# Performance work log

Hardware: AMD Instinct MI355X
Metric: run time of the kernel (lower is better)

The kernel has to match this reference:

```python
import jax, jax.numpy as jnp
import numpy as np

B, C, H, P, DIM, DEPTH, HEADS, MLP, NCLS = 32, 3, 224, 16, 768, 12, 12, 3072, 1000
HD = DIM // HEADS
GRID = H // P  # 14
SEQ = GRID * GRID + 1  # 197
EPS = 1e-6


def _ln(x, g, b):
    m = jnp.mean(x, axis=-1, keepdims=True)
    v = jnp.mean((x - m) ** 2, axis=-1, keepdims=True)
    return (x - m) * jax.lax.rsqrt(v + EPS) * g + b


def setup_inputs() -> dict:
    key = jax.random.key(0)
    ks = jax.random.split(key, 8)
    s = 0.02
    return {
        "img": jax.random.normal(ks[0], (B, C, H, H), dtype=jnp.float32),
        "conv_w": jax.random.normal(ks[1], (DIM, C, P, P), dtype=jnp.float32) * s,
        "conv_b": jnp.zeros((DIM,), jnp.float32),
        "cls_token": jnp.zeros((1, 1, DIM), jnp.float32),
        "pos_emb": jax.random.normal(ks[2], (1, SEQ, DIM), dtype=jnp.float32) * s,
        "ln1_g": jnp.ones((DEPTH, DIM), jnp.float32),
        "ln1_b": jnp.zeros((DEPTH, DIM), jnp.float32),
        "qkv_w": jax.random.normal(ks[3], (DEPTH, 3 * DIM, DIM), dtype=jnp.float32) * s,
        "qkv_b": jnp.zeros((DEPTH, 3 * DIM), jnp.float32),
        "out_w": jax.random.normal(ks[4], (DEPTH, DIM, DIM), dtype=jnp.float32) * s,
        "out_b": jnp.zeros((DEPTH, DIM), jnp.float32),
        "ln2_g": jnp.ones((DEPTH, DIM), jnp.float32),
        "ln2_b": jnp.zeros((DEPTH, DIM), jnp.float32),
        "mlp_w1": jax.random.normal(ks[5], (DEPTH, MLP, DIM), dtype=jnp.float32) * s,
        "mlp_b1": jnp.zeros((DEPTH, MLP), jnp.float32),
        "mlp_w2": jax.random.normal(ks[6], (DEPTH, DIM, MLP), dtype=jnp.float32) * s,
        "mlp_b2": jnp.zeros((DEPTH, DIM), jnp.float32),
        "lnf_g": jnp.ones((DIM,), jnp.float32),
        "lnf_b": jnp.zeros((DIM,), jnp.float32),
        "fc_w": jax.random.normal(ks[7], (NCLS, DIM), dtype=jnp.float32) * s,
        "fc_b": jnp.zeros((NCLS,), jnp.float32),
    }


def reference(img, conv_w, conv_b, cls_token, pos_emb, ln1_g, ln1_b, qkv_w, qkv_b,
              out_w, out_b, ln2_g, ln2_b, mlp_w1, mlp_b1, mlp_w2, mlp_b2,
              lnf_g, lnf_b, fc_w, fc_b):
    b = img.shape[0]
    # Patch embedding: Conv2d(k=P, s=P) == non-overlapping patch matmul.
    patches = img.reshape(b, C, GRID, P, GRID, P)
    x = jnp.einsum('bchpwq,dcpq->bhwd', patches, conv_w).reshape(b, GRID * GRID, DIM) + conv_b
    # prepend CLS, add positional embedding (dropout = identity at eval).
    cls = jnp.broadcast_to(cls_token, (b, 1, DIM))
    x = jnp.concatenate([cls, x], axis=1) + pos_emb[:, :SEQ]

    scale = 1.0 / jnp.sqrt(jnp.float32(HD))

    def layer(x, p):
        g1, b1, qw, qb, ow, ob, g2, b2, w1, bb1, w2, bb2 = p
        h = _ln(x, g1, b1)
        qkv = h @ qw.T + qb                                   # [b,s,3*dim]
        qkv = qkv.reshape(b, SEQ, 3, HEADS, HD)
        q, k, v = [jnp.transpose(qkv[:, :, i], (0, 2, 1, 3)) for i in range(3)]  # [b,h,s,d]
        attn = jax.nn.softmax(jnp.einsum('bhsd,bhtd->bhst', q, k) * scale, axis=-1)
        o = jnp.einsum('bhst,bhtd->bhsd', attn, v)
        o = jnp.transpose(o, (0, 2, 1, 3)).reshape(b, SEQ, DIM)
        x = x + (o @ ow.T + ob)
        h = _ln(x, g2, b2)
        m = jax.nn.gelu(h @ w1.T + bb1, approximate=False) @ w2.T + bb2
        return x + m, None

    x, _ = jax.lax.scan(layer, x, (ln1_g, ln1_b, qkv_w, qkv_b, out_w, out_b,
                                   ln2_g, ln2_b, mlp_w1, mlp_b1, mlp_w2, mlp_b2))
    x = _ln(x, lnf_g, lnf_b)
    return x[:, 0] @ fc_w.T + fc_b
```

## Files before the change

### kernel.cpp

```cpp
#include <hip/hip_runtime.h>
#include <math.h>

#define B_     32
#define SEQ_   197
#define DIM_   768
#define HEADS_ 12
#define HD_    64
#define MLP_   3072
#define NCLS_  1000
#define DEPTH_ 12
#define MROWS  (B_ * SEQ_)
#define MPAD   6400

#define WOFF_QKV 0
#define WOFF_OUT 1769472
#define WOFF_M1  2359296
#define WOFF_M2  4718592
#define LW_      7077888

typedef short s8v __attribute__((ext_vector_type(8)));
typedef float f4v __attribute__((ext_vector_type(4)));

__device__ __forceinline__ unsigned short f2bf(float f) {
    union { float f; unsigned u; } v; v.f = f;
    unsigned r = v.u + 0x7FFFu + ((v.u >> 16) & 1u);
    return (unsigned short)(r >> 16);
}
__device__ __forceinline__ float bf2f(unsigned short h) {
    union { unsigned u; float f; } v; v.u = ((unsigned)h) << 16; return v.f;
}
__device__ __forceinline__ void async16(const void* g, void* l) {
    __builtin_amdgcn_global_load_lds(
        (const __attribute__((address_space(1))) void*)g,
        (__attribute__((address_space(3))) void*)l, 16, 0, 0);
}

enum { EPI_QKV = 0, EPI_RES = 1, EPI_GELU = 2 };

template <int EPI, bool WB>
__global__ __launch_bounds__(256)
void gemm_bf16(const unsigned short* __restrict__ A, const void* __restrict__ Wv,
               const float* __restrict__ bias, float* __restrict__ X,
               unsigned short* __restrict__ O, int M, int N, int K,
               unsigned short* __restrict__ qo, unsigned short* __restrict__ ko,
               unsigned short* __restrict__ vo) {
    __shared__ __align__(16) unsigned short As[128 * 64];
    __shared__ __align__(16) unsigned short Bs[128 * 64];
    const int tid = threadIdx.x;
    const int m0 = blockIdx.y * 128, n0 = blockIdx.x * 128;
    const int w = tid >> 6, lane = tid & 63;
    const int wm = w & 1, wn = w >> 1;
    const int qd = lane >> 4, mr = lane & 15;

    f4v acc[4][4] = {};

    for (int k0 = 0; k0 < K; k0 += 64) {
#pragma unroll
        for (int r = 0; r < 4; r++) {
            int c = r * 256 + tid;
            int m = c >> 3, slot = c & 7;
            int j = slot ^ (m & 7);
            async16(A + (size_t)(m0 + m) * K + k0 + j * 8, (char*)As + c * 16);
        }
        if constexpr (WB) {
            const unsigned short* Wb = (const unsigned short*)Wv;
#pragma unroll
            for (int r = 0; r < 4; r++) {
                int c = r * 256 + tid;
                int n = c >> 3, slot = c & 7;
                int j = slot ^ (n & 7);
                async16(Wb + (size_t)(n0 + n) * K + k0 + j * 8, (char*)Bs + c * 16);
            }
        } else {
            const float* Wf = (const float*)Wv;
#pragma unroll
            for (int r = 0; r < 8; r++) {
                int u = r * 256 + tid;
                int n = u >> 4, kq = (u & 15) * 4;
                const float4 wv = *(const float4*)&Wf[(size_t)(n0 + n) * K + k0 + kq];
                int off = n * 128 + (((kq >> 3) ^ (n & 7)) << 4) + (kq & 7) * 2;
                unsigned p0 = (unsigned)f2bf(wv.x) | ((unsigned)f2bf(wv.y) << 16);
                unsigned p1 = (unsigned)f2bf(wv.z) | ((unsigned)f2bf(wv.w) << 16);
                *(uint2*)((char*)Bs + off) = make_uint2(p0, p1);
            }
        }
        __syncthreads();
#pragma unroll
        for (int s = 0; s < 2; s++) {
            s8v a[4], b[4];
            const int j = s * 4 + qd;
#pragma unroll
            for (int i = 0; i < 4; i++) {
                int ml = wm * 64 + i * 16 + mr;
                a[i] = *(const s8v*)((const char*)As + ml * 128 + ((j ^ (ml & 7)) << 4));
                int nl = wn * 64 + i * 16 + mr;
                b[i] = *(const s8v*)((const char*)Bs + nl * 128 + ((j ^ (nl & 7)) << 4));
            }
#pragma unroll
            for (int i = 0; i < 4; i++)
#pragma unroll
                for (int jj = 0; jj < 4; jj++)
                    acc[i][jj] = __builtin_amdgcn_mfma_f32_16x16x32_bf16(
                        a[i], b[jj], acc[i][jj], 0, 0, 0);
        }
        __syncthreads();
    }

#pragma unroll
    for (int i = 0; i < 4; i++) {
#pragma unroll
        for (int jj = 0; jj < 4; jj++) {
            const int n = n0 + wn * 64 + jj * 16 + mr;
            const float bn = bias[n];
#pragma unroll
            for (int r = 0; r < 4; r++) {
                const int m = m0 + wm * 64 + i * 16 + qd * 4 + r;
                if (m >= M) continue;
                float val = acc[i][jj][r] + bn;
                if constexpr (EPI == EPI_RES) {
                    X[(size_t)m * N + n] += val;
                } else if constexpr (EPI == EPI_GELU) {
                    O[(size_t)m * N + n] =
                        f2bf(0.5f * val * (1.f + erff(val * 0.70710678118654752f)));
                } else {
                    int b = m / SEQ_, s = m - b * SEQ_;
                    int i3 = n / DIM_, nr = n - i3 * DIM_;
                    int hh = nr >> 6, d = nr & 63;
                    unsigned short* dst = (i3 == 0) ? qo : (i3 == 1) ? ko : vo;
                    dst[(((size_t)(b * HEADS_ + hh)) * SEQ_ + s) * HD_ + d] = f2bf(val);
                }
            }
        }
    }
}

__global__ __launch_bounds__(256)
void attention_mfma(const unsigned short* __restrict__ q, const unsigned short* __restrict__ k,
                    const unsigned short* __restrict__ v, unsigned short* __restrict__ ob) {
    __shared__ __align__(16) char smem[59648];
    unsigned short* KV = (unsigned short*)smem;
    unsigned short* P  = (unsigned short*)(smem + 29952);
    const int bh = blockIdx.x, sblk = blockIdx.y;
    const int bi = bh / HEADS_, hh = bh - bi * HEADS_;
    const unsigned short* qp = q + (size_t)bh * SEQ_ * HD_;
    const unsigned short* kp = k + (size_t)bh * SEQ_ * HD_;
    const unsigned short* vp = v + (size_t)bh * SEQ_ * HD_;
    unsigned short* op = ob + (size_t)bi * SEQ_ * DIM_ + hh * HD_;
    const int tid = threadIdx.x;
    const int w = tid >> 6, lane = tid & 63;
    const int mq = lane & 15, quad = lane >> 4;

    for (int c = tid; c < 197 * 8; c += 256) {
        int t = c >> 3, ch = c & 7;
        *(uint4*)(KV + t * 72 + ch * 8) = *(const uint4*)(kp + c * 8);
    }
    if (tid < 88) {
        int t = 197 + (tid >> 3), ch = tid & 7;
        *(uint4*)(KV + t * 72 + ch * 8) = make_uint4(0, 0, 0, 0);
    }
    const int sA = sblk * 64 + w * 16 + mq;
    s8v a0 = *(const s8v*)(qp + sA * 64 + quad * 8);
    s8v a1 = *(const s8v*)(qp + sA * 64 + 32 + quad * 8);
    __syncthreads();

    f4v acc[13] = {};
#pragma unroll
    for (int ti = 0; ti < 13; ti++) {
        const unsigned short* kr = KV + (ti * 16 + mq) * 72 + quad * 8;
        s8v b0 = *(const s8v*)kr;
        s8v b1 = *(const s8v*)(kr + 32);
        acc[ti] = __builtin_amdgcn_mfma_f32_16x16x32_bf16(a0, b0, acc[ti], 0, 0, 0);
        acc[ti] = __builtin_amdgcn_mfma_f32_16x16x32_bf16(a1, b1, acc[ti], 0, 0, 0);
    }
    float mxr[4] = {-3e38f, -3e38f, -3e38f, -3e38f};
#pragma unroll
    for (int ti = 0; ti < 13; ti++) {
        const bool msk = (ti == 12) && (mq >= 5);
#pragma unroll
        for (int r = 0; r < 4; r++) {
            float vs = msk ? -3e38f : acc[ti][r] * 0.125f;
            acc[ti][r] = vs;
            mxr[r] = fmaxf(mxr[r], vs);
        }
    }
#pragma unroll
    for (int r = 0; r < 4; r++)
#pragma unroll
        for (int off = 1; off < 16; off <<= 1)
            mxr[r] = fmaxf(mxr[r], __shfl_xor(mxr[r], off));
    float sum[4] = {0.f, 0.f, 0.f, 0.f};
#pragma unroll
    for (int ti = 0; ti < 13; ti++)
#pragma unroll
        for (int r = 0; r < 4; r++) {
            float e = __expf(acc[ti][r] - mxr[r]);
            acc[ti][r] = e;
            sum[r] += e;
        }
#pragma unroll
    for (int r = 0; r < 4; r++) {
#pragma unroll
        for (int off = 1; off < 16; off <<= 1) sum[r] += __shfl_xor(sum[r], off);
        sum[r] = 1.f / sum[r];
    }
    unsigned short* Pw = P + w * 16 * 232;
#pragma unroll
    for (int ti = 0; ti < 13; ti++)
#pragma unroll
        for (int r = 0; r < 4; r++)
            Pw[(quad * 4 + r) * 232 + ti * 16 + mq] = f2bf(acc[ti][r] * sum[r]);
    {
        int r2 = lane >> 2, c2 = 208 + (lane & 3) * 4;
        *(uint2*)(Pw + r2 * 232 + c2) = make_uint2(0, 0);
    }
    __syncthreads();
    for (int c = tid; c < 197 * 64; c += 256) {
        int t = c >> 6, d = c & 63;
        KV[d * 232 + t] = vp[c];
    }
    for (int c = tid; c < 27 * 64; c += 256) {
        int t = 197 + (c >> 6), d = c & 63;
        KV[d * 232 + t] = 0;
    }
    __syncthreads();
    f4v po[4] = {};
#pragma unroll
    for (int kt = 0; kt < 7; kt++) {
        s8v pa = *(const s8v*)(Pw + mq * 232 + kt * 32 + quad * 8);
#pragma unroll
        for (int nt = 0; nt < 4; nt++) {
            s8v vb2 = *(const s8v*)(KV + (nt * 16 + mq) * 232 + kt * 32 + quad * 8);
            po[nt] = __builtin_amdgcn_mfma_f32_16x16x32_bf16(pa, vb2, po[nt], 0, 0, 0);
        }
    }
#pragma unroll
    for (int nt = 0; nt < 4; nt++)
#pragma unroll
        for (int r = 0; r < 4; r++) {
            int s = sblk * 64 + w * 16 + quad * 4 + r;
            if (s < SEQ_) op[(size_t)s * DIM_ + nt * 16 + mq] = f2bf(po[nt][r]);
        }
}

__global__ __launch_bounds__(256)
void patch_embed_mfma(const unsigned short* __restrict__ imgb,
                      const unsigned short* __restrict__ cwb,
                      const float* __restrict__ cb, const float* __restrict__ pos,
                      float* __restrict__ x) {
    __shared__ __align__(16) unsigned short As[128 * 64];
    __shared__ __align__(16) unsigned short Bs[128 * 64];
    const int tid = threadIdx.x;
    const int m0 = blockIdx.y * 128, n0 = blockIdx.x * 128;
    const int w = tid >> 6, lane = tid & 63;
    const int wm = w & 1, wn = w >> 1;
    const int qd = lane >> 4, mr = lane & 15;

    int rowoff[4], jj4[4];
#pragma unroll
    for (int r = 0; r < 4; r++) {
        int c = r * 256 + tid;
        int m = c >> 3, slot = c & 7;
        jj4[r] = slot ^ (m & 7);
        int mg = m0 + m;
        int b = mg / 196, pp = mg - b * 196;
        int gh = pp / 14, gw = pp - gh * 14;
        rowoff[r] = ((b * 3) * 224 + gh * 16) * 224 + gw * 16;
    }
    f4v acc[4][4] = {};
    for (int k0 = 0; k0 < 768; k0 += 64) {
#pragma unroll
        for (int r = 0; r < 4; r++) {
            int c = r * 256 + tid;
            int kb = k0 + jj4[r] * 8;
            int cc = kb >> 8, rr = (kb >> 4) & 15, qh = kb & 15;
            async16(imgb + rowoff[r] + (cc * 224 + rr) * 224 + qh, (char*)As + c * 16);
        }
#pragma unroll
        for (int r = 0; r < 4; r++) {
            int c = r * 256 + tid;
            int n = c >> 3, slot = c & 7;
            int j = slot ^ (n & 7);
            async16(cwb + (size_t)(n0 + n) * 768 + k0 + j * 8, (char*)Bs + c * 16);
        }
        __syncthreads();
#pragma unroll
        for (int s = 0; s < 2; s++) {
            s8v a[4], b[4];
            const int j = s * 4 + qd;
#pragma unroll
            for (int i = 0; i < 4; i++) {
                int ml = wm * 64 + i * 16 + mr;
                a[i] = *(const s8v*)((const char*)As + ml * 128 + ((j ^ (ml & 7)) << 4));
                int nl = wn * 64 + i * 16 + mr;
                b[i] = *(const s8v*)((const char*)Bs + nl * 128 + ((j ^ (nl & 7)) << 4));
            }
#pragma unroll
            for (int i = 0; i < 4; i++)
#pragma unroll
                for (int jj = 0; jj < 4; jj++)
                    acc[i][jj] = __builtin_amdgcn_mfma_f32_16x16x32_bf16(
                        a[i], b[jj], acc[i][jj], 0, 0, 0);
        }
        __syncthreads();
    }
#pragma unroll
    for (int i = 0; i < 4; i++)
#pragma unroll
        for (int jj = 0; jj < 4; jj++) {
            const int n = n0 + wn * 64 + jj * 16 + mr;
            const float bn = cb[n];
#pragma unroll
            for (int r = 0; r < 4; r++) {
                const int m = m0 + wm * 64 + i * 16 + qd * 4 + r;
                int b = m / 196, pp = m - b * 196;
                x[((size_t)(b * 197 + 1 + pp)) * 768 + n] =
                    acc[i][jj][r] + bn + pos[(size_t)(1 + pp) * 768 + n];
            }
        }
}

#define BM 128
#define BN 64
#define BK 16
__launch_bounds__(256)
__global__ void patch_embed(const float* __restrict__ img, const float* __restrict__ cw,
                            const float* __restrict__ cb, const float* __restrict__ pos,
                            float* __restrict__ x) {
    __shared__ __align__(16) float As[BK][BM + 4];
    __shared__ __align__(16) float Ws[BK][BN + 4];
    const int tid = threadIdx.x;
    const int tx = tid & 15, ty = tid >> 4;
    const int m0 = blockIdx.y * BM;
    const int n0 = blockIdx.x * BN;
    float acc[8][4];
#pragma unroll
    for (int i = 0; i < 8; i++)
#pragma unroll
        for (int j = 0; j < 4; j++) acc[i][j] = 0.f;

    for (int k0 = 0; k0 < 768; k0 += BK) {
#pragma unroll
        for (int it = 0; it < 2; it++) {
            int e4 = tid + it * 256;
            int ml = e4 >> 2;
            int kl = (e4 & 3) * 4;
            int m = m0 + ml;
            int b = m / 196, pp = m - b * 196;
            int gh = pp / 14, gw = pp - gh * 14;
            int k = k0 + kl;
            int c = k >> 8, r = (k >> 4) & 15, qq = k & 15;
            const float4 val = *(const float4*)
                &img[(((size_t)(b * 3 + c) * 224) + gh * 16 + r) * 224 + gw * 16 + qq];
            As[kl + 0][ml] = val.x; As[kl + 1][ml] = val.y;
            As[kl + 2][ml] = val.z; As[kl + 3][ml] = val.w;
        }
        {
            int nl = tid >> 2;
            int kl = (tid & 3) * 4;
            const float4 val = *(const float4*)&cw[(size_t)(n0 + nl) * 768 + k0 + kl];
            Ws[kl + 0][nl] = val.x; Ws[kl + 1][nl] = val.y;
            Ws[kl + 2][nl] = val.z; Ws[kl + 3][nl] = val.w;
        }
        __syncthreads();
#pragma unroll
        for (int kk = 0; kk < BK; kk++) {
            float4 a0 = *(const float4*)&As[kk][ty * 8];
            float4 a1 = *(const float4*)&As[kk][ty * 8 + 4];
            float4 w0 = *(const float4*)&Ws[kk][tx * 4];
            float av[8] = {a0.x, a0.y, a0.z, a0.w, a1.x, a1.y, a1.z, a1.w};
            float wv[4] = {w0.x, w0.y, w0.z, w0.w};
#pragma unroll
            for (int i = 0; i < 8; i++)
#pragma unroll
                for (int j = 0; j < 4; j++) acc[i][j] += av[i] * wv[j];
        }
        __syncthreads();
    }
#pragma unroll
    for (int i = 0; i < 8; i++) {
        int m = m0 + ty * 8 + i;
        int b = m / 196, pp = m - b * 196;
        size_t row = (size_t)b * SEQ_ + 1 + pp;
#pragma unroll
        for (int j = 0; j < 4; j++) {
            int n = n0 + tx * 4 + j;
            x[row * DIM_ + n] = acc[i][j] + cb[n] + pos[(size_t)(1 + pp) * DIM_ + n];
        }
    }
}

__launch_bounds__(256)
__global__ void gemm_f32_bias(const float* __restrict__ A, const float* __restrict__ W,
                              const float* __restrict__ bias, float* __restrict__ C,
                              int M, int N, int K) {
    __shared__ __align__(16) float As[BK][BM + 4];
    __shared__ __align__(16) float Ws[BK][BN + 4];
    const int tid = threadIdx.x;
    const int tx = tid & 15, ty = tid >> 4;
    const int m0 = blockIdx.y * BM;
    const int n0 = blockIdx.x * BN;
    float acc[8][4];
#pragma unroll
    for (int i = 0; i < 8; i++)
#pragma unroll
        for (int j = 0; j < 4; j++) acc[i][j] = 0.f;

    for (int k0 = 0; k0 < K; k0 += BK) {
#pragma unroll
        for (int it = 0; it < 2; it++) {
            int e4 = tid + it * 256;
            int ml = e4 >> 2;
            int kl = (e4 & 3) * 4;
            int m = m0 + ml;
            float4 val = make_float4(0.f, 0.f, 0.f, 0.f);
            if (m < M) val = *(const float4*)&A[(size_t)m * K + k0 + kl];
            As[kl + 0][ml] = val.x; As[kl + 1][ml] = val.y;
            As[kl + 2][ml] = val.z; As[kl + 3][ml] = val.w;
        }
        {
            int nl = tid >> 2;
            int kl = (tid & 3) * 4;
            int n = n0 + nl;
            float4 val = make_float4(0.f, 0.f, 0.f, 0.f);
            if (n < N) val = *(const float4*)&W[(size_t)n * K + k0 + kl];
            Ws[kl + 0][nl] = val.x; Ws[kl + 1][nl] = val.y;
            Ws[kl + 2][nl] = val.z; Ws[kl + 3][nl] = val.w;
        }
        __syncthreads();
#pragma unroll
        for (int kk = 0; kk < BK; kk++) {
            float4 a0 = *(const float4*)&As[kk][ty * 8];
            float4 a1 = *(const float4*)&As[kk][ty * 8 + 4];
            float4 w0 = *(const float4*)&Ws[kk][tx * 4];
            float av[8] = {a0.x, a0.y, a0.z, a0.w, a1.x, a1.y, a1.z, a1.w};
            float wv[4] = {w0.x, w0.y, w0.z, w0.w};
#pragma unroll
            for (int i = 0; i < 8; i++)
#pragma unroll
                for (int j = 0; j < 4; j++) acc[i][j] += av[i] * wv[j];
        }
        __syncthreads();
    }
#pragma unroll
    for (int i = 0; i < 8; i++) {
        int m = m0 + ty * 8 + i;
        if (m >= M) continue;
#pragma unroll
        for (int j = 0; j < 4; j++) {
            int n = n0 + tx * 4 + j;
            if (n >= N) continue;
            C[(size_t)m * N + n] = acc[i][j] + bias[n];
        }
    }
}

__global__ void cls_init(const float* __restrict__ cls, const float* __restrict__ pos,
                         float* __restrict__ x) {
    int idx = blockIdx.x * 256 + threadIdx.x;
    if (idx >= B_ * DIM_) return;
    int b = idx / DIM_, d = idx - b * DIM_;
    x[(size_t)b * SEQ_ * DIM_ + d] = cls[d] + pos[d];
}

template <typename OT>
__global__ __launch_bounds__(256)
void layernorm(const float* __restrict__ in, const float* __restrict__ g,
               const float* __restrict__ bta, OT* __restrict__ out, int row_mul) {
    const float* xr = in + (size_t)blockIdx.x * row_mul * DIM_;
    OT* orow = out + (size_t)blockIdx.x * DIM_;
    int tid = threadIdx.x;
    float v0 = xr[tid], v1 = xr[tid + 256], v2 = xr[tid + 512];
    __shared__ float s1[256], s2[256];
    s1[tid] = v0 + v1 + v2;
    s2[tid] = v0 * v0 + v1 * v1 + v2 * v2;
    __syncthreads();
    for (int off = 128; off > 0; off >>= 1) {
        if (tid < off) { s1[tid] += s1[tid + off]; s2[tid] += s2[tid + off]; }
        __syncthreads();
    }
    float mean = s1[0] * (1.f / 768.f);
    float var = s2[0] * (1.f / 768.f) - mean * mean;
    float rstd = rsqrtf(var + 1e-6f);
#pragma unroll
    for (int c = 0; c < 3; c++) {
        int idx = tid + c * 256;
        float vv = (c == 0) ? v0 : (c == 1) ? v1 : v2;
        float val = (vv - mean) * rstd * g[idx] + bta[idx];
        if constexpr (sizeof(OT) == 2) orow[idx] = f2bf(val);
        else                           orow[idx] = val;
    }
}

__global__ __launch_bounds__(256)
void cvt_weights(const float* __restrict__ qkv, const float* __restrict__ ow,
                 const float* __restrict__ m1, const float* __restrict__ m2,
                 unsigned short* __restrict__ dst) {
    const int L = blockIdx.y;
    const size_t r = ((size_t)blockIdx.x * 256 + threadIdx.x) * 8;
    const float* src;
    if (r < WOFF_OUT)       src = qkv + (size_t)L * 1769472 + r;
    else if (r < WOFF_M1)   src = ow  + (size_t)L * 589824  + (r - WOFF_OUT);
    else if (r < WOFF_M2)   src = m1  + (size_t)L * 2359296 + (r - WOFF_M1);
    else                    src = m2  + (size_t)L * 2359296 + (r - WOFF_M2);
    float4 a = *(const float4*)src, b = *(const float4*)(src + 4);
    unsigned short o[8] = {f2bf(a.x), f2bf(a.y), f2bf(a.z), f2bf(a.w),
                           f2bf(b.x), f2bf(b.y), f2bf(b.z), f2bf(b.w)};
    *(uint4*)(dst + (size_t)L * LW_ + r) = *(uint4*)o;
}

__global__ __launch_bounds__(256)
void cvt_simple(const float* __restrict__ src, unsigned short* __restrict__ dst, int n) {
    int i = (blockIdx.x * 256 + threadIdx.x) * 8;
    if (i >= n) return;
    float4 a = *(const float4*)(src + i), b = *(const float4*)(src + i + 4);
    unsigned short o[8] = {f2bf(a.x), f2bf(a.y), f2bf(a.z), f2bf(a.w),
                           f2bf(b.x), f2bf(b.y), f2bf(b.z), f2bf(b.w)};
    *(uint4*)(dst + i) = *(uint4*)o;
}

extern "C" void kernel_launch(void* const* d_in, const int* in_sizes, int n_in,
                              void* d_out, int out_size, void* d_ws, size_t ws_size,
                              hipStream_t stream) {
    const float* img     = (const float*)d_in[0];
    const float* conv_w  = (const float*)d_in[1];
    const float* conv_b  = (const float*)d_in[2];
    const float* cls_tok = (const float*)d_in[3];
    const float* pos_emb = (const float*)d_in[4];
    const float* ln1_g   = (const float*)d_in[5];
    const float* ln1_b   = (const float*)d_in[6];
    const float* qkv_w   = (const float*)d_in[7];
    const float* qkv_b   = (const float*)d_in[8];
    const float* out_w   = (const float*)d_in[9];
    const float* out_b   = (const float*)d_in[10];
    const float* ln2_g   = (const float*)d_in[11];
    const float* ln2_b   = (const float*)d_in[12];
    const float* mlp_w1  = (const float*)d_in[13];
    const float* mlp_b1  = (const float*)d_in[14];
    const float* mlp_w2  = (const float*)d_in[15];
    const float* mlp_b2  = (const float*)d_in[16];
    const float* lnf_g   = (const float*)d_in[17];
    const float* lnf_b   = (const float*)d_in[18];
    const float* fc_w    = (const float*)d_in[19];
    const float* fc_b    = (const float*)d_in[20];
    float* out = (float*)d_out;

    char* p = (char*)d_ws;
    float* x = (float*)p;                      p += (size_t)MROWS * DIM_ * 4;
    unsigned short* h    = (unsigned short*)p; p += (size_t)MPAD * DIM_ * 2;
    unsigned short* qb   = (unsigned short*)p; p += (size_t)MROWS * DIM_ * 2;
    unsigned short* kb   = (unsigned short*)p; p += (size_t)MROWS * DIM_ * 2;
    unsigned short* vb   = (unsigned short*)p; p += (size_t)MROWS * DIM_ * 2;
    unsigned short* obuf = (unsigned short*)p; p += (size_t)MPAD * DIM_ * 2;
    unsigned short* mid  = (unsigned short*)p; p += (size_t)MPAD * MLP_ * 2;
    float* hcls = (float*)p;                   p += (size_t)B_ * DIM_ * 4;
    unsigned short* imgb = (unsigned short*)p; p += (size_t)B_ * 3 * 224 * 224 * 2;
    unsigned short* cwb  = (unsigned short*)p; p += (size_t)DIM_ * DIM_ * 2;
    unsigned short* wall = (unsigned short*)p; p += (size_t)DEPTH_ * LW_ * 2;

    const bool full = ws_size >= 288178176ull;
    dim3 blk(256);

    if (full) {
        cvt_simple<<<2352, blk, 0, stream>>>(img, imgb, B_ * 3 * 224 * 224);
        cvt_simple<<<288, blk, 0, stream>>>(conv_w, cwb, DIM_ * DIM_);
        cvt_weights<<<dim3(3456, DEPTH_), blk, 0, stream>>>(qkv_w, out_w, mlp_w1, mlp_w2, wall);
        patch_embed_mfma<<<dim3(6, 49), blk, 0, stream>>>(imgb, cwb, conv_b, pos_emb, x);
    } else {
        patch_embed<<<dim3(12, 49), blk, 0, stream>>>(img, conv_w, conv_b, pos_emb, x);
    }
    cls_init<<<(B_ * DIM_ + 255) / 256, blk, 0, stream>>>(cls_tok, pos_emb, x);

    const int MT = (MROWS + 127) / 128;
    for (int L = 0; L < DEPTH_; L++) {
        const unsigned short* wl = wall + (size_t)L * LW_;
        layernorm<unsigned short><<<MROWS, blk, 0, stream>>>(
            x, ln1_g + L * DIM_, ln1_b + L * DIM_, h, 1);
        if (full)
            gemm_bf16<EPI_QKV, true><<<dim3(3 * DIM_ / 128, MT), blk, 0, stream>>>(
                h, wl + WOFF_QKV, qkv_b + (size_t)L * 3 * DIM_,
                nullptr, nullptr, MROWS, 3 * DIM_, DIM_, qb, kb, vb);
        else
            gemm_bf16<EPI_QKV, false><<<dim3(3 * DIM_ / 128, MT), blk, 0, stream>>>(
                h, qkv_w + (size_t)L * 3 * DIM_ * DIM_, qkv_b + (size_t)L * 3 * DIM_,
                nullptr, nullptr, MROWS, 3 * DIM_, DIM_, qb, kb, vb);
        attention_mfma<<<dim3(B_ * HEADS_, 4), blk, 0, stream>>>(qb, kb, vb, obuf);
        if (full)
            gemm_bf16<EPI_RES, true><<<dim3(DIM_ / 128, MT), blk, 0, stream>>>(
                obuf, wl + WOFF_OUT, out_b + (size_t)L * DIM_,
                x, nullptr, MROWS, DIM_, DIM_, nullptr, nullptr, nullptr);
        else
            gemm_bf16<EPI_RES, false><<<dim3(DIM_ / 128, MT), blk, 0, stream>>>(
                obuf, out_w + (size_t)L * DIM_ * DIM_, out_b + (size_t)L * DIM_,
                x, nullptr, MROWS, DIM_, DIM_, nullptr, nullptr, nullptr);
        layernorm<unsigned short><<<MROWS, blk, 0, stream>>>(
            x, ln2_g + L * DIM_, ln2_b + L * DIM_, h, 1);
        if (full)
            gemm_bf16<EPI_GELU, true><<<dim3(MLP_ / 128, MT), blk, 0, stream>>>(
                h, wl + WOFF_M1, mlp_b1 + (size_t)L * MLP_,
                nullptr, mid, MROWS, MLP_, DIM_, nullptr, nullptr, nullptr);
        else
            gemm_bf16<EPI_GELU, false><<<dim3(MLP_ / 128, MT), blk, 0, stream>>>(
                h, mlp_w1 + (size_t)L * MLP_ * DIM_, mlp_b1 + (size_t)L * MLP_,
                nullptr, mid, MROWS, MLP_, DIM_, nullptr, nullptr, nullptr);
        if (full)
            gemm_bf16<EPI_RES, true><<<dim3(DIM_ / 128, MT), blk, 0, stream>>>(
                mid, wl + WOFF_M2, mlp_b2 + (size_t)L * DIM_,
                x, nullptr, MROWS, DIM_, MLP_, nullptr, nullptr, nullptr);
        else
            gemm_bf16<EPI_RES, false><<<dim3(DIM_ / 128, MT), blk, 0, stream>>>(
                mid, mlp_w2 + (size_t)L * DIM_ * MLP_, mlp_b2 + (size_t)L * DIM_,
                x, nullptr, MROWS, DIM_, MLP_, nullptr, nullptr, nullptr);
    }
    layernorm<float><<<B_, blk, 0, stream>>>(x, lnf_g, lnf_b, hcls, SEQ_);
    gemm_f32_bias<<<dim3((NCLS_ + BN - 1) / BN, 1), blk, 0, stream>>>(
        hcls, fc_w, fc_b, out, B_, NCLS_, DIM_);
}
```

Baseline: 3.894 ms.

## Template GEMM tile sizes, warp-per-row layernorm, swizzled V transpose, fold attention scale

```diff
diff --git a/kernel.cpp b/kernel.cpp
--- a/kernel.cpp
+++ b/kernel.cpp
@@ -37,26 +37,26 @@
 
 enum { EPI_QKV = 0, EPI_RES = 1, EPI_GELU = 2 };
 
-template <int EPI, bool WB>
+template <int EPI, bool WB, int FM, int FN>
 __global__ __launch_bounds__(256)
 void gemm_bf16(const unsigned short* __restrict__ A, const void* __restrict__ Wv,
                const float* __restrict__ bias, float* __restrict__ X,
                unsigned short* __restrict__ O, int M, int N, int K,
                unsigned short* __restrict__ qo, unsigned short* __restrict__ ko,
                unsigned short* __restrict__ vo) {
-    __shared__ __align__(16) unsigned short As[128 * 64];
-    __shared__ __align__(16) unsigned short Bs[128 * 64];
+    __shared__ __align__(16) unsigned short As[32 * FM * 64];
+    __shared__ __align__(16) unsigned short Bs[32 * FN * 64];
     const int tid = threadIdx.x;
-    const int m0 = blockIdx.y * 128, n0 = blockIdx.x * 128;
+    const int m0 = blockIdx.y * (32 * FM), n0 = blockIdx.x * (32 * FN);
     const int w = tid >> 6, lane = tid & 63;
     const int wm = w & 1, wn = w >> 1;
     const int qd = lane >> 4, mr = lane & 15;
 
-    f4v acc[4][4] = {};
+    f4v acc[FM][FN] = {};
 
     for (int k0 = 0; k0 < K; k0 += 64) {
 #pragma unroll
-        for (int r = 0; r < 4; r++) {
+        for (int r = 0; r < FM; r++) {
             int c = r * 256 + tid;
             int m = c >> 3, slot = c & 7;
             int j = slot ^ (m & 7);
@@ -65,7 +65,7 @@
         if constexpr (WB) {
             const unsigned short* Wb = (const unsigned short*)Wv;
 #pragma unroll
-            for (int r = 0; r < 4; r++) {
+            for (int r = 0; r < FN; r++) {
                 int c = r * 256 + tid;
                 int n = c >> 3, slot = c & 7;
                 int j = slot ^ (n & 7);
@@ -74,7 +74,7 @@
         } else {
             const float* Wf = (const float*)Wv;
 #pragma unroll
-            for (int r = 0; r < 8; r++) {
+            for (int r = 0; r < 2 * FN; r++) {
                 int u = r * 256 + tid;
                 int n = u >> 4, kq = (u & 15) * 4;
                 const float4 wv = *(const float4*)&Wf[(size_t)(n0 + n) * K + k0 + kq];
@@ -87,19 +87,22 @@
         __syncthreads();
 #pragma unroll
         for (int s = 0; s < 2; s++) {
-            s8v a[4], b[4];
+            s8v a[FM], b[FN];
             const int j = s * 4 + qd;
 #pragma unroll
-            for (int i = 0; i < 4; i++) {
-                int ml = wm * 64 + i * 16 + mr;
+            for (int i = 0; i < FM; i++) {
+                int ml = wm * 16 * FM + i * 16 + mr;
                 a[i] = *(const s8v*)((const char*)As + ml * 128 + ((j ^ (ml & 7)) << 4));
-                int nl = wn * 64 + i * 16 + mr;
+            }
+#pragma unroll
+            for (int i = 0; i < FN; i++) {
+                int nl = wn * 16 * FN + i * 16 + mr;
                 b[i] = *(const s8v*)((const char*)Bs + nl * 128 + ((j ^ (nl & 7)) << 4));
             }
 #pragma unroll
-            for (int i = 0; i < 4; i++)
-#pragma unroll
-                for (int jj = 0; jj < 4; jj++)
+            for (int i = 0; i < FM; i++)
+#pragma unroll
+                for (int jj = 0; jj < FN; jj++)
                     acc[i][jj] = __builtin_amdgcn_mfma_f32_16x16x32_bf16(
                         a[i], b[jj], acc[i][jj], 0, 0, 0);
         }
@@ -107,14 +110,14 @@
     }
 
 #pragma unroll
-    for (int i = 0; i < 4; i++) {
-#pragma unroll
-        for (int jj = 0; jj < 4; jj++) {
-            const int n = n0 + wn * 64 + jj * 16 + mr;
+    for (int i = 0; i < FM; i++) {
+#pragma unroll
+        for (int jj = 0; jj < FN; jj++) {
+            const int n = n0 + wn * 16 * FN + jj * 16 + mr;
             const float bn = bias[n];
 #pragma unroll
             for (int r = 0; r < 4; r++) {
-                const int m = m0 + wm * 64 + i * 16 + qd * 4 + r;
+                const int m = m0 + wm * 16 * FM + i * 16 + qd * 4 + r;
                 if (m >= M) continue;
                 float val = acc[i][jj][r] + bn;
                 if constexpr (EPI == EPI_RES) {
@@ -126,6 +129,7 @@
                     int b = m / SEQ_, s = m - b * SEQ_;
                     int i3 = n / DIM_, nr = n - i3 * DIM_;
                     int hh = nr >> 6, d = nr & 63;
+                    if (i3 == 0) val *= 0.125f;
                     unsigned short* dst = (i3 == 0) ? qo : (i3 == 1) ? ko : vo;
                     dst[(((size_t)(b * HEADS_ + hh)) * SEQ_ + s) * HD_ + d] = f2bf(val);
                 }
@@ -137,9 +141,9 @@
 __global__ __launch_bounds__(256)
 void attention_mfma(const unsigned short* __restrict__ q, const unsigned short* __restrict__ k,
                     const unsigned short* __restrict__ v, unsigned short* __restrict__ ob) {
-    __shared__ __align__(16) char smem[59648];
+    __shared__ __align__(16) char smem[62464];
     unsigned short* KV = (unsigned short*)smem;
-    unsigned short* P  = (unsigned short*)(smem + 29952);
+    unsigned short* P  = (unsigned short*)(smem + 32768);
     const int bh = blockIdx.x, sblk = blockIdx.y;
     const int bi = bh / HEADS_, hh = bh - bi * HEADS_;
     const unsigned short* qp = q + (size_t)bh * SEQ_ * HD_;
@@ -178,7 +182,7 @@
         const bool msk = (ti == 12) && (mq >= 5);
 #pragma unroll
         for (int r = 0; r < 4; r++) {
-            float vs = msk ? -3e38f : acc[ti][r] * 0.125f;
+            float vs = msk ? -3e38f : acc[ti][r];
             acc[ti][r] = vs;
             mxr[r] = fmaxf(mxr[r], vs);
         }
@@ -214,13 +218,30 @@
         *(uint2*)(Pw + r2 * 232 + c2) = make_uint2(0, 0);
     }
     __syncthreads();
-    for (int c = tid; c < 197 * 64; c += 256) {
-        int t = c >> 6, d = c & 63;
-        KV[d * 232 + t] = vp[c];
-    }
-    for (int c = tid; c < 27 * 64; c += 256) {
-        int t = 197 + (c >> 6), d = c & 63;
-        KV[d * 232 + t] = 0;
+#pragma unroll
+    for (int pass = 0; pass < 2; pass++) {
+        int u = pass * 256 + tid;
+        int o = u & 7;
+        int tq = u >> 3;
+        uint4 rv[4];
+#pragma unroll
+        for (int tt = 0; tt < 4; tt++) {
+            int t = tq * 4 + tt;
+            rv[tt] = (t < SEQ_) ? *(const uint4*)(vp + t * 64 + o * 8)
+                                : make_uint4(0, 0, 0, 0);
+        }
+#pragma unroll
+        for (int i = 0; i < 8; i++) {
+            int d = o * 8 + i;
+            int cs = (tq >> 1) ^ i ^ o;
+            unsigned short p0 = ((const unsigned short*)&rv[0])[i];
+            unsigned short p1 = ((const unsigned short*)&rv[1])[i];
+            unsigned short p2 = ((const unsigned short*)&rv[2])[i];
+            unsigned short p3 = ((const unsigned short*)&rv[3])[i];
+            uint2 w2 = make_uint2((unsigned)p0 | ((unsigned)p1 << 16),
+                                  (unsigned)p2 | ((unsigned)p3 << 16));
+            *(uint2*)((char*)KV + d * 512 + cs * 16 + (tq & 1) * 8) = w2;
+        }
     }
     __syncthreads();
     f4v po[4] = {};
@@ -229,7 +250,9 @@
         s8v pa = *(const s8v*)(Pw + mq * 232 + kt * 32 + quad * 8);
 #pragma unroll
         for (int nt = 0; nt < 4; nt++) {
-            s8v vb2 = *(const s8v*)(KV + (nt * 16 + mq) * 232 + kt * 32 + quad * 8);
+            int d = nt * 16 + mq;
+            int cs = (kt * 4 + quad) ^ (d & 7) ^ ((d >> 3) & 7);
+            s8v vb2 = *(const s8v*)((const char*)KV + d * 512 + cs * 16);
             po[nt] = __builtin_amdgcn_mfma_f32_16x16x32_bf16(pa, vb2, po[nt], 0, 0, 0);
         }
     }
@@ -464,30 +487,45 @@
 
 template <typename OT>
 __global__ __launch_bounds__(256)
-void layernorm(const float* __restrict__ in, const float* __restrict__ g,
-               const float* __restrict__ bta, OT* __restrict__ out, int row_mul) {
-    const float* xr = in + (size_t)blockIdx.x * row_mul * DIM_;
-    OT* orow = out + (size_t)blockIdx.x * DIM_;
-    int tid = threadIdx.x;
-    float v0 = xr[tid], v1 = xr[tid + 256], v2 = xr[tid + 512];
-    __shared__ float s1[256], s2[256];
-    s1[tid] = v0 + v1 + v2;
-    s2[tid] = v0 * v0 + v1 * v1 + v2 * v2;
-    __syncthreads();
-    for (int off = 128; off > 0; off >>= 1) {
-        if (tid < off) { s1[tid] += s1[tid + off]; s2[tid] += s2[tid + off]; }
-        __syncthreads();
-    }
-    float mean = s1[0] * (1.f / 768.f);
-    float var = s2[0] * (1.f / 768.f) - mean * mean;
-    float rstd = rsqrtf(var + 1e-6f);
-#pragma unroll
-    for (int c = 0; c < 3; c++) {
-        int idx = tid + c * 256;
-        float vv = (c == 0) ? v0 : (c == 1) ? v1 : v2;
-        float val = (vv - mean) * rstd * g[idx] + bta[idx];
-        if constexpr (sizeof(OT) == 2) orow[idx] = f2bf(val);
-        else                           orow[idx] = val;
+void layernorm_w(const float* __restrict__ in, const float* __restrict__ g,
+                 const float* __restrict__ bta, OT* __restrict__ out,
+                 int rows, int row_mul) {
+    const int w = threadIdx.x >> 6, lane = threadIdx.x & 63;
+    const int row = blockIdx.x * 4 + w;
+    if (row >= rows) return;
+    const float* xr = in + (size_t)row * row_mul * DIM_;
+    float4 v[3];
+    float s = 0.f, s2 = 0.f;
+#pragma unroll
+    for (int j = 0; j < 3; j++) {
+        v[j] = *(const float4*)&xr[lane * 4 + j * 256];
+        s  += v[j].x + v[j].y + v[j].z + v[j].w;
+        s2 += v[j].x * v[j].x + v[j].y * v[j].y + v[j].z * v[j].z + v[j].w * v[j].w;
+    }
+#pragma unroll
+    for (int off = 32; off > 0; off >>= 1) {
+        s += __shfl_xor(s, off);
+        s2 += __shfl_xor(s2, off);
+    }
+    const float mean = s * (1.f / 768.f);
+    const float var = s2 * (1.f / 768.f) - mean * mean;
+    const float rstd = rsqrtf(var + 1e-6f);
+    OT* orow = out + (size_t)row * DIM_;
+#pragma unroll
+    for (int j = 0; j < 3; j++) {
+        const int c = lane * 4 + j * 256;
+        const float4 gv = *(const float4*)&g[c];
+        const float4 bv = *(const float4*)&bta[c];
+        float r0 = (v[j].x - mean) * rstd * gv.x + bv.x;
+        float r1 = (v[j].y - mean) * rstd * gv.y + bv.y;
+        float r2 = (v[j].z - mean) * rstd * gv.z + bv.z;
+        float r3 = (v[j].w - mean) * rstd * gv.w + bv.w;
+        if constexpr (sizeof(OT) == 2) {
+            unsigned short pk[4] = {f2bf(r0), f2bf(r1), f2bf(r2), f2bf(r3)};
+            *(uint2*)&orow[c] = *(const uint2*)pk;
+        } else {
+            *(float4*)&orow[c] = make_float4(r0, r1, r2, r3);
+        }
     }
 }
 
@@ -570,48 +608,50 @@
     }
     cls_init<<<(B_ * DIM_ + 255) / 256, blk, 0, stream>>>(cls_tok, pos_emb, x);
 
-    const int MT = (MROWS + 127) / 128;
+    const int MT  = (MROWS + 127) / 128;
+    const int MT2 = (MROWS + 63) / 64;
+    const int LNB = (MROWS + 3) / 4;
     for (int L = 0; L < DEPTH_; L++) {
         const unsigned short* wl = wall + (size_t)L * LW_;
-        layernorm<unsigned short><<<MROWS, blk, 0, stream>>>(
-            x, ln1_g + L * DIM_, ln1_b + L * DIM_, h, 1);
+        layernorm_w<unsigned short><<<LNB, blk, 0, stream>>>(
+            x, ln1_g + L * DIM_, ln1_b + L * DIM_, h, MROWS, 1);
         if (full)
-            gemm_bf16<EPI_QKV, true><<<dim3(3 * DIM_ / 128, MT), blk, 0, stream>>>(
+            gemm_bf16<EPI_QKV, true, 4, 4><<<dim3(18, MT), blk, 0, stream>>>(
                 h, wl + WOFF_QKV, qkv_b + (size_t)L * 3 * DIM_,
                 nullptr, nullptr, MROWS, 3 * DIM_, DIM_, qb, kb, vb);
         else
-            gemm_bf16<EPI_QKV, false><<<dim3(3 * DIM_ / 128, MT), blk, 0, stream>>>(
+            gemm_bf16<EPI_QKV, false, 4, 4><<<dim3(18, MT), blk, 0, stream>>>(
                 h, qkv_w + (size_t)L * 3 * DIM_ * DIM_, qkv_b + (size_t)L * 3 * DIM_,
                 nullptr, nullptr, MROWS, 3 * DIM_, DIM_, qb, kb, vb);
         attention_mfma<<<dim3(B_ * HEADS_, 4), blk, 0, stream>>>(qb, kb, vb, obuf);
         if (full)
-            gemm_bf16<EPI_RES, true><<<dim3(DIM_ / 128, MT), blk, 0, stream>>>(
+            gemm_bf16<EPI_RES, true, 2, 4><<<dim3(6, MT2), blk, 0, stream>>>(
                 obuf, wl + WOFF_OUT, out_b + (size_t)L * DIM_,
                 x, nullptr, MROWS, DIM_, DIM_, nullptr, nullptr, nullptr);
         else
-            gemm_bf16<EPI_RES, false><<<dim3(DIM_ / 128, MT), blk, 0, stream>>>(
+            gemm_bf16<EPI_RES, false, 2, 4><<<dim3(6, MT2), blk, 0, stream>>>(
                 obuf, out_w + (size_t)L * DIM_ * DIM_, out_b + (size_t)L * DIM_,
                 x, nullptr, MROWS, DIM_, DIM_, nullptr, nullptr, nullptr);
-        layernorm<unsigned short><<<MROWS, blk, 0, stream>>>(
-            x, ln2_g + L * DIM_, ln2_b + L * DIM_, h, 1);
+        layernorm_w<unsigned short><<<LNB, blk, 0, stream>>>(
+            x, ln2_g + L * DIM_, ln2_b + L * DIM_, h, MROWS, 1);
         if (full)
-            gemm_bf16<EPI_GELU, true><<<dim3(MLP_ / 128, MT), blk, 0, stream>>>(
+            gemm_bf16<EPI_GELU, true, 4, 4><<<dim3(24, MT), blk, 0, stream>>>(
                 h, wl + WOFF_M1, mlp_b1 + (size_t)L * MLP_,
                 nullptr, mid, MROWS, MLP_, DIM_, nullptr, nullptr, nullptr);
         else
-            gemm_bf16<EPI_GELU, false><<<dim3(MLP_ / 128, MT), blk, 0, stream>>>(
+            gemm_bf16<EPI_GELU, false, 4, 4><<<dim3(24, MT), blk, 0, stream>>>(
                 h, mlp_w1 + (size_t)L * MLP_ * DIM_, mlp_b1 + (size_t)L * MLP_,
                 nullptr, mid, MROWS, MLP_, DIM_, nullptr, nullptr, nullptr);
         if (full)
-            gemm_bf16<EPI_RES, true><<<dim3(DIM_ / 128, MT), blk, 0, stream>>>(
+            gemm_bf16<EPI_RES, true, 2, 4><<<dim3(6, MT2), blk, 0, stream>>>(
                 mid, wl + WOFF_M2, mlp_b2 + (size_t)L * DIM_,
                 x, nullptr, MROWS, DIM_, MLP_, nullptr, nullptr, nullptr);
         else
-            gemm_bf16<EPI_RES, false><<<dim3(DIM_ / 128, MT), blk, 0, stream>>>(
+            gemm_bf16<EPI_RES, false, 2, 4><<<dim3(6, MT2), blk, 0, stream>>>(
                 mid, mlp_w2 + (size_t)L * DIM_ * MLP_, mlp_b2 + (size_t)L * DIM_,
                 x, nullptr, MROWS, DIM_, MLP_, nullptr, nullptr, nullptr);
     }
-    layernorm<float><<<B_, blk, 0, stream>>>(x, lnf_g, lnf_b, hcls, SEQ_);
+    layernorm_w<float><<<8, blk, 0, stream>>>(x, lnf_g, lnf_b, hcls, B_, SEQ_);
     gemm_f32_bias<<<dim3((NCLS_ + BN - 1) / BN, 1), blk, 0, stream>>>(
         hcls, fc_w, fc_b, out, B_, NCLS_, DIM_);
 }
```

Result: faster. 3.320 ms (-14.7%).
